# Kernel optimization log

Measured on AMD Instinct MI355X. Metric: run time of the kernel, lower is better.

The kernel has to match this reference:

```python
import jax, jax.numpy as jnp
import numpy as np

D_MODEL = 512
NUM_HEADS = 8
DEPTH = D_MODEL // NUM_HEADS
BATCH = 16
SEQ = 1024


def setup_inputs() -> dict:
    key = jax.random.key(0)
    kq, kk, kv, k1, k2, k3, k4 = jax.random.split(key, 7)
    scale = 1.0 / np.sqrt(D_MODEL)
    return {
        "v": jax.random.normal(kv, (BATCH, SEQ, D_MODEL), jnp.float32),
        "k": jax.random.normal(kk, (BATCH, SEQ, D_MODEL), jnp.float32),
        "q": jax.random.normal(kq, (BATCH, SEQ, D_MODEL), jnp.float32),
        "mask": jnp.ones((BATCH, SEQ), jnp.float32),
        # Conv1D(kernel_size=1, use_bias=False) == per-token Linear: x @ W, W [d_in, d_out]
        "Wq": jax.random.normal(k1, (D_MODEL, D_MODEL), jnp.float32) * scale,
        "Wk": jax.random.normal(k2, (D_MODEL, D_MODEL), jnp.float32) * scale,
        "Wv": jax.random.normal(k3, (D_MODEL, D_MODEL), jnp.float32) * scale,
        "Wo": jax.random.normal(k4, (D_MODEL, D_MODEL), jnp.float32) * scale,
    }


def _split_heads(x, batch):
    # [b, s, d_model] -> [b, h, s, depth]
    return x.reshape(batch, -1, NUM_HEADS, DEPTH).transpose(0, 2, 1, 3)


def reference(v, k, q, mask, Wq, Wk, Wv, Wo):
    batch = q.shape[0]
    qh = _split_heads(q @ Wq, batch)  # [b,h,sq,dh]
    kh = _split_heads(k @ Wk, batch)  # [b,h,sk,dh]
    vh = _split_heads(v @ Wv, batch)  # [b,h,sk,dh]

    dk = jnp.asarray(DEPTH, qh.dtype)
    logits = jnp.einsum("bhqd,bhkd->bhqk", qh, kh) / jnp.sqrt(dk)
    # additive padding mask, broadcast [b,1,1,sk]
    logits = logits + (1.0 - mask[:, None, None, :]) * (-1e9)
    attention_weights = jax.nn.softmax(logits, axis=-1)  # [b,h,sq,sk]

    ctx = jnp.einsum("bhqk,bhkd->bhqd", attention_weights, vh)
    ctx = ctx.transpose(0, 2, 1, 3).reshape(batch, -1, D_MODEL)
    output = ctx @ Wo
    return output, attention_weights
```

## Files before the change

kernel.cpp:

```cpp
#include <hip/hip_runtime.h>


typedef _Float16 f16;
typedef _Float16 f16x8 __attribute__((ext_vector_type(8)));
typedef _Float16 f16x4 __attribute__((ext_vector_type(4)));
typedef float f32x4 __attribute__((ext_vector_type(4)));

#define DEVINL __device__ __forceinline__

static constexpr int BATCH = 16, SEQ = 1024, DM = 512, NH = 8, DH = 64;

DEVINL void async16(void* lds, const void* g) {
  __builtin_amdgcn_global_load_lds(
      (const __attribute__((address_space(1))) unsigned int*)g,
      (__attribute__((address_space(3))) unsigned int*)lds, 16, 0, 0);
}

__global__ __launch_bounds__(256) void prep_wt_k(
    const float* __restrict__ Wq, const float* __restrict__ Wk,
    const float* __restrict__ Wv, const float* __restrict__ Wo,
    f16* __restrict__ WT) {
  __shared__ float t[32][33];
  const int w = blockIdx.z;
  const float* src = (w == 0) ? Wq : (w == 1) ? Wk : (w == 2) ? Wv : Wo;
  const int k0 = blockIdx.y * 32, n0 = blockIdx.x * 32;
  const int r0 = threadIdx.x >> 5, c = threadIdx.x & 31;
#pragma unroll
  for (int i = 0; i < 4; ++i)
    t[i * 8 + r0][c] = src[(size_t)(k0 + i * 8 + r0) * DM + n0 + c];
  __syncthreads();
  f16* dst = WT + (size_t)w * DM * DM;
#pragma unroll
  for (int i = 0; i < 4; ++i)
    dst[(size_t)(n0 + i * 8 + r0) * DM + k0 + c] = (f16)t[c][i * 8 + r0];
}

template <int MODE>
DEVINL void gemm_body(const float* __restrict__ A32, const f16* __restrict__ A16,
                      const f16* __restrict__ WTn, f16* __restrict__ O16,
                      float* __restrict__ O32, int m0, int n0, bool vt) {
  __shared__ __align__(16) f16 As[2][128 * 32];
  __shared__ __align__(16) f16 Bs[2][128 * 32];
  const int tid = threadIdx.x;
  const int lane = tid & 63, wave = tid >> 6;
  const int wr = wave >> 1, wc = wave & 1;
  const int lrow = lane & 15, lkg = lane >> 4;
  f32x4 acc[4][4] = {};

  f32x4 ar[4];

  auto stageB = [&](int kt, int buf) {
#pragma unroll
    for (int it = 0; it < 2; ++it) {
      const int o = (it * 256 + tid) * 16;
      const int n = o >> 6, kb = o & 63;
      async16((char*)&Bs[buf][0] + (it * 256 + wave * 64) * 16,
              (const char*)WTn + ((size_t)(n0 + n) * DM + kt * 32) * 2 + kb);
    }
  };
  auto stageA_async = [&](int kt, int buf) {
#pragma unroll
    for (int it = 0; it < 2; ++it) {
      const int o = (it * 256 + tid) * 16;
      const int row = o >> 6, kb = o & 63;
      async16((char*)&As[buf][0] + (it * 256 + wave * 64) * 16,
              (const char*)A16 + ((size_t)(m0 + row) * DM + kt * 32) * 2 + kb);
    }
  };
  auto loadA = [&](int kt) {
#pragma unroll
    for (int c = 0; c < 4; ++c) {
      const int idx = c * 256 + tid;
      const int row = idx >> 3, sub = idx & 7;
      ar[c] = *(const f32x4*)(A32 + (size_t)(m0 + row) * DM + kt * 32 + sub * 4);
    }
  };
  auto writeA = [&](int buf) {
#pragma unroll
    for (int c = 0; c < 4; ++c) {
      const int idx = c * 256 + tid;
      const int row = idx >> 3, sub = idx & 7;
      f16x4 t;
      t[0] = (f16)ar[c][0]; t[1] = (f16)ar[c][1];
      t[2] = (f16)ar[c][2]; t[3] = (f16)ar[c][3];
      *(f16x4*)&As[buf][row * 32 + sub * 4] = t;
    }
  };

  stageB(0, 0);
  if (MODE == 0) {
    loadA(0);
    writeA(0);
  } else {
    stageA_async(0, 0);
  }
  __syncthreads();

  for (int kt = 0; kt < DM / 32; ++kt) {
    const int cur = kt & 1;
    if (kt < DM / 32 - 1) {
      stageB(kt + 1, cur ^ 1);
      if (MODE == 0) loadA(kt + 1);
      else stageA_async(kt + 1, cur ^ 1);
    }
    f16x8 af[4], bf[4];
#pragma unroll
    for (int i = 0; i < 4; ++i)
      af[i] = *(const f16x8*)&As[cur][(wr * 64 + i * 16 + lrow) * 32 + lkg * 8];
#pragma unroll
    for (int j = 0; j < 4; ++j)
      bf[j] = *(const f16x8*)&Bs[cur][(wc * 64 + j * 16 + lrow) * 32 + lkg * 8];
#pragma unroll
    for (int i = 0; i < 4; ++i)
#pragma unroll
      for (int j = 0; j < 4; ++j)
        acc[i][j] = __builtin_amdgcn_mfma_f32_16x16x32_f16(af[i], bf[j], acc[i][j], 0, 0, 0);
    if (MODE == 0 && kt < DM / 32 - 1) writeA(cur ^ 1);
    __syncthreads();
  }

#pragma unroll
  for (int i = 0; i < 4; ++i) {
#pragma unroll
    for (int j = 0; j < 4; ++j) {
#pragma unroll
      for (int r = 0; r < 4; ++r) {
        const int m = m0 + wr * 64 + i * 16 + lkg * 4 + r;
        const int g = n0 + wc * 64 + j * 16 + lrow;
        if (MODE == 0) {
          const int b = m >> 10, s = m & 1023, hh = g >> 6, d = g & 63;
          if (vt)
            O16[(((size_t)b * NH + hh) * DH + d) * SEQ + s] = (f16)acc[i][j][r];
          else
            O16[(((size_t)b * NH + hh) * SEQ + s) * DH + d] = (f16)acc[i][j][r];
        } else {
          O32[(size_t)m * DM + g] = acc[i][j][r];
        }
      }
    }
  }
}

__global__ __launch_bounds__(256, 2) void proj_k(
    const float* __restrict__ q, const float* __restrict__ k, const float* __restrict__ v,
    const f16* __restrict__ WT, f16* __restrict__ Qh, f16* __restrict__ Kh,
    f16* __restrict__ Vh) {
  const int bid = blockIdx.x;
  const int wid = (bid & 7) * 192 + (bid >> 3);
  const int n_blk = wid & 3, m_blk = (wid >> 2) & 127, z = wid >> 9;
  const float* A = (z == 0) ? q : (z == 1) ? k : v;
  const f16* W = WT + (size_t)z * DM * DM;
  f16* O = (z == 0) ? Qh : (z == 1) ? Kh : Vh;
  gemm_body<0>(A, nullptr, W, O, nullptr, m_blk * 128, n_blk * 128, z == 2);
}

__global__ __launch_bounds__(256, 2) void outp_k(const f16* __restrict__ ctx,
                                                 const f16* __restrict__ WoT,
                                                 float* __restrict__ out0) {
  const int bid = blockIdx.x;
  const int wid = (bid & 7) * 64 + (bid >> 3);
  const int n_blk = wid & 3, m_blk = wid >> 2;
  gemm_body<1>(nullptr, ctx, WoT, nullptr, out0, m_blk * 128, n_blk * 128, false);
}

__global__ __launch_bounds__(256, 3) void attn_k(
    const f16* __restrict__ Qh, const f16* __restrict__ Kh, const f16* __restrict__ VTh,
    const float* __restrict__ mask, float* __restrict__ attnW, f16* __restrict__ ctx) {
  __shared__ __align__(16) f16 Ks[2][64 * 64];
  __shared__ __align__(16) f16 Vt[2][64 * 64];
  __shared__ __align__(16) f16 Ps[4][16 * 64];
  __shared__ __align__(16) float Ms[SEQ];
  const int tid = threadIdx.x;
  const int lane = tid & 63, wave = tid >> 6;
  const int lq = lane & 15, g = lane >> 4;
  const int bid = blockIdx.x;
  const int wid = (bid & 7) * 256 + (bid >> 3);
  const int qt = wid & 15, h = (wid >> 4) & 7, b = wid >> 7;
  const size_t bh = (size_t)b * NH + h;
  const char* Kbase = (const char*)(Kh + bh * SEQ * DH);
  const char* VTbase = (const char*)(VTh + bh * (size_t)DH * SEQ);
  const int q0 = qt * 64 + wave * 16;

  auto stageK = [&](int kt, int buf) {
    const char* KtileB = Kbase + (size_t)kt * 64 * DH * 2;
#pragma unroll
    for (int it = 0; it < 2; ++it) {
      const int o = (it * 256 + tid) * 16;
      const int key = o >> 7, slot = (o >> 4) & 7;
      async16((char*)&Ks[buf][0] + (it * 256 + wave * 64) * 16,
              KtileB + key * 128 + ((slot ^ (key & 7)) << 4));
    }
  };
  auto stageV = [&](int kt, int buf) {
    const char* VtileB = VTbase + (size_t)kt * 64 * 2;
#pragma unroll
    for (int it = 0; it < 2; ++it) {
      const int o = (it * 256 + tid) * 16;
      const int d = o >> 7, slot = (o >> 4) & 7;
      async16((char*)&Vt[buf][0] + (it * 256 + wave * 64) * 16,
              VtileB + (size_t)d * (SEQ * 2) + ((slot ^ (d & 7)) << 4));
    }
  };

  {
    f32x4 mv = *(const f32x4*)(mask + (size_t)b * SEQ + tid * 4);
    f32x4 bv;
    bv[0] = (1.0f - mv[0]) * (-1e9f);
    bv[1] = (1.0f - mv[1]) * (-1e9f);
    bv[2] = (1.0f - mv[2]) * (-1e9f);
    bv[3] = (1.0f - mv[3]) * (-1e9f);
    *(f32x4*)&Ms[tid * 4] = bv;
  }

  f16x8 aQ0, aQ1;
  {
    const f16* qp = Qh + (bh * SEQ + q0 + lq) * DH + g * 8;
    aQ0 = *(const f16x8*)qp;
    aQ1 = *(const f16x8*)(qp + 32);
  }

  stageK(0, 0);
  __syncthreads();
  float ssum = 0.0f;
  for (int kt = 0; kt < 16; ++kt) {
    const int cur = kt & 1;
    if (kt < 15) stageK(kt + 1, cur ^ 1);
    f32x4 lg[4] = {};
#pragma unroll
    for (int j = 0; j < 4; ++j) {
      const int krow = j * 16 + lq;
      f16x8 a0 = *(const f16x8*)((const char*)&Ks[cur][0] + krow * 128 + ((g ^ (krow & 7)) << 4));
      f16x8 a1 = *(const f16x8*)((const char*)&Ks[cur][0] + krow * 128 + (((4 + g) ^ (krow & 7)) << 4));
      lg[j] = __builtin_amdgcn_mfma_f32_16x16x32_f16(a0, aQ0, lg[j], 0, 0, 0);
      lg[j] = __builtin_amdgcn_mfma_f32_16x16x32_f16(a1, aQ1, lg[j], 0, 0, 0);
    }
#pragma unroll
    for (int j = 0; j < 4; ++j) {
      f32x4 bias = *(const f32x4*)&Ms[kt * 64 + j * 16 + g * 4];
#pragma unroll
      for (int r = 0; r < 4; ++r) ssum += __expf(lg[j][r] * 0.125f + bias[r]);
    }
    __syncthreads();
  }

  ssum += __shfl_xor(ssum, 16);
  ssum += __shfl_xor(ssum, 32);
  const float inv = 1.0f / ssum;

  f32x4 ctxacc[4] = {};
  f32x4 wbuf[4][4];
  float* awBase = attnW + (bh * SEQ + q0) * SEQ;

  stageK(0, 0);
  stageV(0, 0);
  __syncthreads();
  for (int kt4 = 0; kt4 < 4; ++kt4) {
#pragma unroll
    for (int u = 0; u < 4; ++u) {
      const int kt = kt4 * 4 + u;
      const int cur = kt & 1;
      if (kt < 15) {
        stageK(kt + 1, cur ^ 1);
        stageV(kt + 1, cur ^ 1);
      }
      f32x4 lg[4] = {};
#pragma unroll
      for (int j = 0; j < 4; ++j) {
        const int krow = j * 16 + lq;
        f16x8 a0 = *(const f16x8*)((const char*)&Ks[cur][0] + krow * 128 + ((g ^ (krow & 7)) << 4));
        f16x8 a1 = *(const f16x8*)((const char*)&Ks[cur][0] + krow * 128 + (((4 + g) ^ (krow & 7)) << 4));
        lg[j] = __builtin_amdgcn_mfma_f32_16x16x32_f16(a0, aQ0, lg[j], 0, 0, 0);
        lg[j] = __builtin_amdgcn_mfma_f32_16x16x32_f16(a1, aQ1, lg[j], 0, 0, 0);
      }
#pragma unroll
      for (int j = 0; j < 4; ++j) {
        f32x4 bias = *(const f32x4*)&Ms[kt * 64 + j * 16 + g * 4];
        f32x4 w;
#pragma unroll
        for (int r = 0; r < 4; ++r) w[r] = __expf(lg[j][r] * 0.125f + bias[r]) * inv;
        wbuf[u][j] = w;
        f16x4 pw;
        pw[0] = (f16)w[0]; pw[1] = (f16)w[1]; pw[2] = (f16)w[2]; pw[3] = (f16)w[3];
        const int slot = 2 * j + (g >> 1);
        *(f16x4*)((char*)&Ps[wave][0] + lq * 128 + ((slot ^ (lq & 7)) << 4) + 8 * (g & 1)) = pw;
      }
#pragma unroll
      for (int kk = 0; kk < 2; ++kk) {
        f16x8 aP = *(const f16x8*)((const char*)&Ps[wave][0] + lq * 128 +
                                   (((4 * kk + g) ^ (lq & 7)) << 4));
#pragma unroll
        for (int j2 = 0; j2 < 4; ++j2) {
          const int drow = j2 * 16 + lq;
          f16x8 bV = *(const f16x8*)((const char*)&Vt[cur][0] + drow * 128 +
                                     (((4 * kk + g) ^ (drow & 7)) << 4));
          ctxacc[j2] = __builtin_amdgcn_mfma_f32_16x16x32_f16(aP, bV, ctxacc[j2], 0, 0, 0);
        }
      }
      if (u == 3) {
        float* awRow = awBase + (size_t)lq * SEQ + kt4 * 256 + g * 4;
#pragma unroll
        for (int jj = 0; jj < 4; ++jj)
#pragma unroll
          for (int j = 0; j < 4; ++j)
            *(f32x4*)(awRow + jj * 64 + j * 16) = wbuf[jj][j];
      }
      __syncthreads();
    }
  }

#pragma unroll
  for (int j2 = 0; j2 < 4; ++j2)
#pragma unroll
    for (int r = 0; r < 4; ++r) {
      const int s = q0 + g * 4 + r;
      const int d = j2 * 16 + lq;
      ctx[(((size_t)b * SEQ + s) * NH + h) * DH + d] = (f16)ctxacc[j2][r];
    }
}

extern "C" void kernel_launch(void* const* d_in, const int* in_sizes, int n_in,
                              void* d_out, int out_size, void* d_ws, size_t ws_size,
                              hipStream_t stream) {
  const float* v = (const float*)d_in[0];
  const float* k = (const float*)d_in[1];
  const float* q = (const float*)d_in[2];
  const float* mask = (const float*)d_in[3];
  const float* Wq = (const float*)d_in[4];
  const float* Wk = (const float*)d_in[5];
  const float* Wv = (const float*)d_in[6];
  const float* Wo = (const float*)d_in[7];

  float* out0 = (float*)d_out;
  float* attnW = out0 + (size_t)BATCH * SEQ * DM;

  char* ws = (char*)d_ws;
  f16* WT = (f16*)ws;
  f16* Qh = (f16*)(ws + (size_t)4 * DM * DM * 2);
  f16* Kh = Qh + (size_t)BATCH * NH * SEQ * DH;
  f16* VTh = Kh + (size_t)BATCH * NH * SEQ * DH;
  f16* ctx = VTh + (size_t)BATCH * NH * SEQ * DH;

  prep_wt_k<<<dim3(16, 16, 4), 256, 0, stream>>>(Wq, Wk, Wv, Wo, WT);
  proj_k<<<dim3(1536), 256, 0, stream>>>(q, k, v, WT, Qh, Kh, VTh);
  attn_k<<<dim3(2048), 256, 0, stream>>>(Qh, Kh, VTh, mask, attnW, ctx);
  outp_k<<<dim3(512), 256, 0, stream>>>(ctx, WT + (size_t)3 * DM * DM, out0);
}
```

Before: 375.7 us.

## Stage attention weights in LDS for coalesced stores, drop K/V double buffering

The attention-weight tile for 256 keys is now buffered in LDS per wave and written back to global memory as full contiguous rows, instead of being held in registers and stored as scattered 16-byte chunks. K/V double buffering is removed to free LDS for the larger per-wave weight buffer, so each tile load is now followed immediately by a barrier with no prefetch overlap. The weights written out are now rounded to fp16 before conversion back to fp32, which reduces the precision of the attention-weight output.

Measured after the change: 339.7 us. 1.11x faster.

```diff
diff --git a/kernel.cpp b/kernel.cpp
--- a/kernel.cpp
+++ b/kernel.cpp
@@ -166,9 +166,9 @@
 __global__ __launch_bounds__(256, 3) void attn_k(
     const f16* __restrict__ Qh, const f16* __restrict__ Kh, const f16* __restrict__ VTh,
     const float* __restrict__ mask, float* __restrict__ attnW, f16* __restrict__ ctx) {
-  __shared__ __align__(16) f16 Ks[2][64 * 64];
-  __shared__ __align__(16) f16 Vt[2][64 * 64];
-  __shared__ __align__(16) f16 Ps[4][16 * 64];
+  __shared__ __align__(16) f16 Ks[64 * 64];
+  __shared__ __align__(16) f16 Vt[64 * 64];
+  __shared__ __align__(16) f16 Pw[4][16 * 256];
   __shared__ __align__(16) float Ms[SEQ];
   const int tid = threadIdx.x;
   const int lane = tid & 63, wave = tid >> 6;
@@ -181,23 +181,23 @@
   const char* VTbase = (const char*)(VTh + bh * (size_t)DH * SEQ);
   const int q0 = qt * 64 + wave * 16;
 
-  auto stageK = [&](int kt, int buf) {
+  auto stageK = [&](int kt) {
     const char* KtileB = Kbase + (size_t)kt * 64 * DH * 2;
 #pragma unroll
     for (int it = 0; it < 2; ++it) {
       const int o = (it * 256 + tid) * 16;
       const int key = o >> 7, slot = (o >> 4) & 7;
-      async16((char*)&Ks[buf][0] + (it * 256 + wave * 64) * 16,
+      async16((char*)Ks + (it * 256 + wave * 64) * 16,
               KtileB + key * 128 + ((slot ^ (key & 7)) << 4));
     }
   };
-  auto stageV = [&](int kt, int buf) {
+  auto stageV = [&](int kt) {
     const char* VtileB = VTbase + (size_t)kt * 64 * 2;
 #pragma unroll
     for (int it = 0; it < 2; ++it) {
       const int o = (it * 256 + tid) * 16;
       const int d = o >> 7, slot = (o >> 4) & 7;
-      async16((char*)&Vt[buf][0] + (it * 256 + wave * 64) * 16,
+      async16((char*)Vt + (it * 256 + wave * 64) * 16,
               VtileB + (size_t)d * (SEQ * 2) + ((slot ^ (d & 7)) << 4));
     }
   };
@@ -219,18 +219,16 @@
     aQ1 = *(const f16x8*)(qp + 32);
   }
 
-  stageK(0, 0);
-  __syncthreads();
   float ssum = 0.0f;
   for (int kt = 0; kt < 16; ++kt) {
-    const int cur = kt & 1;
-    if (kt < 15) stageK(kt + 1, cur ^ 1);
+    stageK(kt);
+    __syncthreads();
     f32x4 lg[4] = {};
 #pragma unroll
     for (int j = 0; j < 4; ++j) {
       const int krow = j * 16 + lq;
-      f16x8 a0 = *(const f16x8*)((const char*)&Ks[cur][0] + krow * 128 + ((g ^ (krow & 7)) << 4));
-      f16x8 a1 = *(const f16x8*)((const char*)&Ks[cur][0] + krow * 128 + (((4 + g) ^ (krow & 7)) << 4));
+      f16x8 a0 = *(const f16x8*)((const char*)Ks + krow * 128 + ((g ^ (krow & 7)) << 4));
+      f16x8 a1 = *(const f16x8*)((const char*)Ks + krow * 128 + (((4 + g) ^ (krow & 7)) << 4));
       lg[j] = __builtin_amdgcn_mfma_f32_16x16x32_f16(a0, aQ0, lg[j], 0, 0, 0);
       lg[j] = __builtin_amdgcn_mfma_f32_16x16x32_f16(a1, aQ1, lg[j], 0, 0, 0);
     }
@@ -248,27 +246,21 @@
   const float inv = 1.0f / ssum;
 
   f32x4 ctxacc[4] = {};
-  f32x4 wbuf[4][4];
   float* awBase = attnW + (bh * SEQ + q0) * SEQ;
 
-  stageK(0, 0);
-  stageV(0, 0);
-  __syncthreads();
   for (int kt4 = 0; kt4 < 4; ++kt4) {
 #pragma unroll
     for (int u = 0; u < 4; ++u) {
       const int kt = kt4 * 4 + u;
-      const int cur = kt & 1;
-      if (kt < 15) {
-        stageK(kt + 1, cur ^ 1);
-        stageV(kt + 1, cur ^ 1);
-      }
+      stageK(kt);
+      stageV(kt);
+      __syncthreads();
       f32x4 lg[4] = {};
 #pragma unroll
       for (int j = 0; j < 4; ++j) {
         const int krow = j * 16 + lq;
-        f16x8 a0 = *(const f16x8*)((const char*)&Ks[cur][0] + krow * 128 + ((g ^ (krow & 7)) << 4));
-        f16x8 a1 = *(const f16x8*)((const char*)&Ks[cur][0] + krow * 128 + (((4 + g) ^ (krow & 7)) << 4));
+        f16x8 a0 = *(const f16x8*)((const char*)Ks + krow * 128 + ((g ^ (krow & 7)) << 4));
+        f16x8 a1 = *(const f16x8*)((const char*)Ks + krow * 128 + (((4 + g) ^ (krow & 7)) << 4));
         lg[j] = __builtin_amdgcn_mfma_f32_16x16x32_f16(a0, aQ0, lg[j], 0, 0, 0);
         lg[j] = __builtin_amdgcn_mfma_f32_16x16x32_f16(a1, aQ1, lg[j], 0, 0, 0);
       }
@@ -278,31 +270,33 @@
         f32x4 w;
 #pragma unroll
         for (int r = 0; r < 4; ++r) w[r] = __expf(lg[j][r] * 0.125f + bias[r]) * inv;
-        wbuf[u][j] = w;
         f16x4 pw;
         pw[0] = (f16)w[0]; pw[1] = (f16)w[1]; pw[2] = (f16)w[2]; pw[3] = (f16)w[3];
-        const int slot = 2 * j + (g >> 1);
-        *(f16x4*)((char*)&Ps[wave][0] + lq * 128 + ((slot ^ (lq & 7)) << 4) + 8 * (g & 1)) = pw;
+        const int s = u * 8 + j * 2 + (g >> 1);
+        *(f16x4*)((char*)&Pw[wave][0] + lq * 512 + (((s ^ (lq & 7)) << 4)) + (g & 1) * 8) = pw;
       }
 #pragma unroll
       for (int kk = 0; kk < 2; ++kk) {
-        f16x8 aP = *(const f16x8*)((const char*)&Ps[wave][0] + lq * 128 +
-                                   (((4 * kk + g) ^ (lq & 7)) << 4));
+        const int s = u * 8 + kk * 4 + g;
+        f16x8 aP = *(const f16x8*)((const char*)&Pw[wave][0] + lq * 512 + ((s ^ (lq & 7)) << 4));
 #pragma unroll
         for (int j2 = 0; j2 < 4; ++j2) {
           const int drow = j2 * 16 + lq;
-          f16x8 bV = *(const f16x8*)((const char*)&Vt[cur][0] + drow * 128 +
+          f16x8 bV = *(const f16x8*)((const char*)Vt + drow * 128 +
                                      (((4 * kk + g) ^ (drow & 7)) << 4));
           ctxacc[j2] = __builtin_amdgcn_mfma_f32_16x16x32_f16(aP, bV, ctxacc[j2], 0, 0, 0);
         }
       }
       if (u == 3) {
-        float* awRow = awBase + (size_t)lq * SEQ + kt4 * 256 + g * 4;
-#pragma unroll
-        for (int jj = 0; jj < 4; ++jj)
-#pragma unroll
-          for (int j = 0; j < 4; ++j)
-            *(f32x4*)(awRow + jj * 64 + j * 16) = wbuf[jj][j];
+#pragma unroll
+        for (int i = 0; i < 16; ++i) {
+          f16x4 pv = *(const f16x4*)((const char*)&Pw[wave][0] + i * 512 +
+                                     (((lane >> 1) ^ (i & 7)) << 4) + (lane & 1) * 8);
+          f32x4 o;
+          o[0] = (float)pv[0]; o[1] = (float)pv[1];
+          o[2] = (float)pv[2]; o[3] = (float)pv[3];
+          *(f32x4*)(awBase + (size_t)i * SEQ + kt4 * 256 + lane * 4) = o;
+        }
       }
       __syncthreads();
     }
```
